# Optimization experiments

Hardware: AMD Instinct MI355X
Metric: run time of the kernel (lower is better)

## Reference

```python
import jax, jax.numpy as jnp
import numpy as np

TEMPERATURE = 0.1

def setup_inputs() -> dict:
    key = jax.random.key(0)
    k1, k2 = jax.random.split(key)
    z_i = jax.random.normal(k1, (4096, 128), dtype=jnp.float32)
    z_j = jax.random.normal(k2, (4096, 128), dtype=jnp.float32)
    return {"z_i": z_i, "z_j": z_j}

def reference(z_i, z_j):
    n = z_i.shape[0]
    reps = jnp.concatenate([z_i, z_j], axis=0)              # (2N, D)
    # cosine similarity via normalize + GEMM (same math as broadcasted CosineSimilarity,
    # torch eps=1e-8 on the norm)
    norms = jnp.maximum(jnp.linalg.norm(reps, axis=1, keepdims=True), 1e-8)
    rn = reps / norms
    sim = rn @ rn.T                                          # (2N, 2N)
    l_pos = jnp.diagonal(sim, offset=n)                      # (N,)
    r_pos = jnp.diagonal(sim, offset=-n)                     # (N,)
    positives = jnp.concatenate([l_pos, r_pos])[:, None]     # (2N, 1)
    # NOTE: original code's mask bug makes `negatives` the FULL sim matrix
    logits = jnp.concatenate([positives, sim], axis=1) / TEMPERATURE  # (2N, 2N+1)
    # cross-entropy with label 0, reduction='sum'
    log_probs = jax.nn.log_softmax(logits, axis=1)
    loss = -jnp.sum(log_probs[:, 0])
    return loss / (2 * n)
```

## Files before the change

### kernel.cpp

```cpp
#include <hip/hip_runtime.h>
#include <hip/hip_bf16.h>

typedef __bf16 bf16x8 __attribute__((ext_vector_type(8)));
typedef __bf16 bf16x2 __attribute__((ext_vector_type(2)));
typedef float f32x4 __attribute__((ext_vector_type(4)));

#define NROWS 8192
#define HALF_N 4096
#define DIM 128
#define ROW_BYTES 256
#define C1 14.42695040888963f
#define LN2 0.6931471805599453f

__global__ __launch_bounds__(256) void k_normalize(
    const float* __restrict__ zi, const float* __restrict__ zj,
    char* __restrict__ rn, char* __restrict__ rnA, float* __restrict__ rowsum)
{
    const int wave = threadIdx.x >> 6;
    const int lane = threadIdx.x & 63;
    #pragma unroll
    for (int i = 0; i < 4; ++i) {
        const int row = blockIdx.x * 16 + wave * 4 + i;
        const float* src = (row < HALF_N) ? (zi + (size_t)row * DIM)
                                          : (zj + (size_t)(row - HALF_N) * DIM);
        float2 v = *(const float2*)(src + lane * 2);
        float ss = v.x * v.x + v.y * v.y;
        #pragma unroll
        for (int m = 32; m >= 1; m >>= 1) ss += __shfl_xor(ss, m, 64);
        const float sc = 1.0f / fmaxf(sqrtf(ss), 1e-8f);
        bf16x2 a, b;
        a[0] = (__bf16)(v.x * sc);      a[1] = (__bf16)(v.y * sc);
        b[0] = (__bf16)(v.x * sc * C1); b[1] = (__bf16)(v.y * sc * C1);
        *(bf16x2*)(rn  + (size_t)row * ROW_BYTES + lane * 4) = a;
        *(bf16x2*)(rnA + (size_t)row * ROW_BYTES + lane * 4) = b;
    }
    if (threadIdx.x < 16) rowsum[blockIdx.x * 16 + threadIdx.x] = 0.0f;
}

__global__ __launch_bounds__(256) void k_gemm(
    const char* __restrict__ rn, const char* __restrict__ rnA,
    float* __restrict__ rowsum)
{
    const int wave = threadIdx.x >> 6;
    const int lane = threadIdx.x & 63;
    const int qrow = lane >> 4, lcol = lane & 15;
    const int cv = blockIdx.x & 15;
    const int rg = (blockIdx.x >> 4) * 4 + wave;

    const char* Ab = rnA + (size_t)(rg * 64) * ROW_BYTES;
    bf16x8 afrag[4][4];
    #pragma unroll
    for (int mi = 0; mi < 4; ++mi)
        #pragma unroll
        for (int ks = 0; ks < 4; ++ks)
            afrag[mi][ks] = *(const bf16x8*)(Ab + (mi * 16 + lcol) * ROW_BYTES
                                             + ks * 64 + qrow * 16);

    float rsum[4][4];
    #pragma unroll
    for (int mi = 0; mi < 4; ++mi)
        #pragma unroll
        for (int r = 0; r < 4; ++r) rsum[mi][r] = 0.0f;

    const char* Bb = rn + (size_t)(cv * 512) * ROW_BYTES + lcol * ROW_BYTES + qrow * 16;

    #pragma unroll 1
    for (int s = 0; s < 32; ++s) {
        const char* bp = Bb + s * 16 * ROW_BYTES;
        bf16x8 bfrag[4];
        #pragma unroll
        for (int ks = 0; ks < 4; ++ks)
            bfrag[ks] = *(const bf16x8*)(bp + ks * 64);

        f32x4 acc[4];
        const f32x4 zero = {0.0f, 0.0f, 0.0f, 0.0f};
        #pragma unroll
        for (int mi = 0; mi < 4; ++mi) acc[mi] = zero;
        #pragma unroll
        for (int ks = 0; ks < 4; ++ks)
            #pragma unroll
            for (int mi = 0; mi < 4; ++mi)
                acc[mi] = __builtin_amdgcn_mfma_f32_16x16x32_bf16(
                    afrag[mi][ks], bfrag[ks], acc[mi], 0, 0, 0);

        #pragma unroll
        for (int mi = 0; mi < 4; ++mi)
            #pragma unroll
            for (int r = 0; r < 4; ++r)
                rsum[mi][r] += __builtin_amdgcn_exp2f(acc[mi][r]);
    }

    #pragma unroll
    for (int mi = 0; mi < 4; ++mi)
        #pragma unroll
        for (int r = 0; r < 4; ++r) {
            float v = rsum[mi][r];
            v += __shfl_xor(v, 1, 64);
            v += __shfl_xor(v, 2, 64);
            v += __shfl_xor(v, 4, 64);
            v += __shfl_xor(v, 8, 64);
            if (lcol == 0)
                atomicAdd(&rowsum[rg * 64 + mi * 16 + qrow * 4 + r], v);
        }
}

__global__ __launch_bounds__(256) void k_rowloss(
    const char* __restrict__ rn, const float* __restrict__ rowsum,
    float* __restrict__ row_loss)
{
    const int row  = blockIdx.x * 4 + (threadIdx.x >> 6);
    const int lane = threadIdx.x & 63;
    const int partner = (row + HALF_N) & (NROWS - 1);
    const bf16x2 a = *(const bf16x2*)(rn + (size_t)row * ROW_BYTES + lane * 4);
    const bf16x2 b = *(const bf16x2*)(rn + (size_t)partner * ROW_BYTES + lane * 4);
    float p = (float)a[0] * (float)b[0] + (float)a[1] * (float)b[1];
    #pragma unroll
    for (int m = 32; m >= 1; m >>= 1) p += __shfl_xor(p, m, 64);
    if (lane == 0) {
        const float pc = p * C1;
        const float S  = rowsum[row] + __builtin_amdgcn_exp2f(pc);
        row_loss[row] = (__builtin_amdgcn_logf(S) - pc) * LN2;
    }
}

__global__ __launch_bounds__(256) void k_reduce(
    const float* __restrict__ row_loss, float* __restrict__ out)
{
    const f32x4* v4 = (const f32x4*)row_loss;
    float s = 0.0f;
    for (int i = threadIdx.x; i < NROWS / 4; i += 256) {
        f32x4 v = v4[i];
        s += (v[0] + v[1]) + (v[2] + v[3]);
    }
    #pragma unroll
    for (int m = 32; m >= 1; m >>= 1) s += __shfl_xor(s, m, 64);
    __shared__ float part[4];
    if ((threadIdx.x & 63) == 0) part[threadIdx.x >> 6] = s;
    __syncthreads();
    if (threadIdx.x == 0)
        out[0] = (part[0] + part[1] + part[2] + part[3]) * (1.0f / (float)NROWS);
}

extern "C" void kernel_launch(void* const* d_in, const int* in_sizes, int n_in,
                              void* d_out, int out_size, void* d_ws, size_t ws_size,
                              hipStream_t stream)
{
    const float* zi = (const float*)d_in[0];
    const float* zj = (const float*)d_in[1];
    float* out = (float*)d_out;

    char*  rn       = (char*)d_ws;
    char*  rnA      = rn + (size_t)NROWS * ROW_BYTES;
    float* rowsum   = (float*)(rnA + (size_t)NROWS * ROW_BYTES);
    float* row_loss = rowsum + NROWS;

    k_normalize<<<NROWS / 16, 256, 0, stream>>>(zi, zj, rn, rnA, rowsum);
    k_gemm<<<512, 256, 0, stream>>>(rn, rnA, rowsum);
    k_rowloss<<<NROWS / 4, 256, 0, stream>>>(rn, rowsum, row_loss);
    k_reduce<<<1, 256, 0, stream>>>(row_loss, out);
}
```

Baseline: 102.9 us.

## Fuse rowloss and reduce into GEMM via last-block pattern, halve GEMM tile

Normalization now processes z_i/z_j row pairs together and computes the positive-pair cosine directly into a buffer, removing the separate rowloss kernel. The GEMM grid doubles to 1024 blocks, each wave handling 32 rows instead of 64, and B fragments are double-buffered across iterations. A global atomic counter lets the last finishing block compute per-row losses and the final mean, eliminating two kernel launches. This trades launch overhead for an atomic fence and a serial tail in one block, and the positive logit now uses fp32 values instead of bf16.

```diff
diff --git a/kernel.cpp b/kernel.cpp
--- a/kernel.cpp
+++ b/kernel.cpp
@@ -11,35 +11,55 @@
 #define ROW_BYTES 256
 #define C1 14.42695040888963f
 #define LN2 0.6931471805599453f
+#define GBLK 1024
 
 __global__ __launch_bounds__(256) void k_normalize(
     const float* __restrict__ zi, const float* __restrict__ zj,
-    char* __restrict__ rn, char* __restrict__ rnA, float* __restrict__ rowsum)
+    char* __restrict__ rn, char* __restrict__ rnA,
+    float* __restrict__ rowsum, float* __restrict__ pbuf,
+    unsigned int* __restrict__ done)
 {
     const int wave = threadIdx.x >> 6;
     const int lane = threadIdx.x & 63;
     #pragma unroll
-    for (int i = 0; i < 4; ++i) {
-        const int row = blockIdx.x * 16 + wave * 4 + i;
-        const float* src = (row < HALF_N) ? (zi + (size_t)row * DIM)
-                                          : (zj + (size_t)(row - HALF_N) * DIM);
-        float2 v = *(const float2*)(src + lane * 2);
-        float ss = v.x * v.x + v.y * v.y;
+    for (int t = 0; t < 2; ++t) {
+        const int idx = blockIdx.x * 8 + wave * 2 + t;
+        float2 vi = *(const float2*)(zi + (size_t)idx * DIM + lane * 2);
+        float2 vj = *(const float2*)(zj + (size_t)idx * DIM + lane * 2);
+        float ssi = vi.x * vi.x + vi.y * vi.y;
+        float ssj = vj.x * vj.x + vj.y * vj.y;
+        float cr  = vi.x * vj.x + vi.y * vj.y;
         #pragma unroll
-        for (int m = 32; m >= 1; m >>= 1) ss += __shfl_xor(ss, m, 64);
-        const float sc = 1.0f / fmaxf(sqrtf(ss), 1e-8f);
+        for (int m = 32; m >= 1; m >>= 1) {
+            ssi += __shfl_xor(ssi, m, 64);
+            ssj += __shfl_xor(ssj, m, 64);
+            cr  += __shfl_xor(cr,  m, 64);
+        }
+        const float sci = 1.0f / fmaxf(sqrtf(ssi), 1e-8f);
+        const float scj = 1.0f / fmaxf(sqrtf(ssj), 1e-8f);
         bf16x2 a, b;
-        a[0] = (__bf16)(v.x * sc);      a[1] = (__bf16)(v.y * sc);
-        b[0] = (__bf16)(v.x * sc * C1); b[1] = (__bf16)(v.y * sc * C1);
-        *(bf16x2*)(rn  + (size_t)row * ROW_BYTES + lane * 4) = a;
-        *(bf16x2*)(rnA + (size_t)row * ROW_BYTES + lane * 4) = b;
+        a[0] = (__bf16)(vi.x * sci);      a[1] = (__bf16)(vi.y * sci);
+        b[0] = (__bf16)(vi.x * sci * C1); b[1] = (__bf16)(vi.y * sci * C1);
+        *(bf16x2*)(rn  + (size_t)idx * ROW_BYTES + lane * 4) = a;
+        *(bf16x2*)(rnA + (size_t)idx * ROW_BYTES + lane * 4) = b;
+        a[0] = (__bf16)(vj.x * scj);      a[1] = (__bf16)(vj.y * scj);
+        b[0] = (__bf16)(vj.x * scj * C1); b[1] = (__bf16)(vj.y * scj * C1);
+        *(bf16x2*)(rn  + (size_t)(idx + HALF_N) * ROW_BYTES + lane * 4) = a;
+        *(bf16x2*)(rnA + (size_t)(idx + HALF_N) * ROW_BYTES + lane * 4) = b;
+        if (lane == 0) {
+            const float p = cr * sci * scj;
+            pbuf[idx] = p;
+            pbuf[idx + HALF_N] = p;
+        }
     }
     if (threadIdx.x < 16) rowsum[blockIdx.x * 16 + threadIdx.x] = 0.0f;
+    if (blockIdx.x == 0 && threadIdx.x == 0) *done = 0u;
 }
 
 __global__ __launch_bounds__(256) void k_gemm(
     const char* __restrict__ rn, const char* __restrict__ rnA,
-    float* __restrict__ rowsum)
+    float* __restrict__ rowsum, const float* __restrict__ pbuf,
+    unsigned int* __restrict__ done, float* __restrict__ out)
 {
     const int wave = threadIdx.x >> 6;
     const int lane = threadIdx.x & 63;
@@ -47,51 +67,69 @@
     const int cv = blockIdx.x & 15;
     const int rg = (blockIdx.x >> 4) * 4 + wave;
 
-    const char* Ab = rnA + (size_t)(rg * 64) * ROW_BYTES;
-    bf16x8 afrag[4][4];
+    const char* Ab = rnA + (size_t)(rg * 32) * ROW_BYTES;
+    bf16x8 afrag[2][4];
     #pragma unroll
-    for (int mi = 0; mi < 4; ++mi)
+    for (int mi = 0; mi < 2; ++mi)
         #pragma unroll
         for (int ks = 0; ks < 4; ++ks)
             afrag[mi][ks] = *(const bf16x8*)(Ab + (mi * 16 + lcol) * ROW_BYTES
                                              + ks * 64 + qrow * 16);
 
-    float rsum[4][4];
+    float rsum[2][4];
     #pragma unroll
-    for (int mi = 0; mi < 4; ++mi)
+    for (int mi = 0; mi < 2; ++mi)
         #pragma unroll
         for (int r = 0; r < 4; ++r) rsum[mi][r] = 0.0f;
 
     const char* Bb = rn + (size_t)(cv * 512) * ROW_BYTES + lcol * ROW_BYTES + qrow * 16;
 
+    bf16x8 b0[4], b1[4];
+    #pragma unroll
+    for (int ks = 0; ks < 4; ++ks) b0[ks] = *(const bf16x8*)(Bb + ks * 64);
+
+    const f32x4 zero = {0.0f, 0.0f, 0.0f, 0.0f};
     #pragma unroll 1
-    for (int s = 0; s < 32; ++s) {
-        const char* bp = Bb + s * 16 * ROW_BYTES;
-        bf16x8 bfrag[4];
+    for (int s = 0; s < 32; s += 2) {
+        const char* bp1 = Bb + (size_t)(s + 1) * 16 * ROW_BYTES;
         #pragma unroll
-        for (int ks = 0; ks < 4; ++ks)
-            bfrag[ks] = *(const bf16x8*)(bp + ks * 64);
+        for (int ks = 0; ks < 4; ++ks) b1[ks] = *(const bf16x8*)(bp1 + ks * 64);
 
-        f32x4 acc[4];
-        const f32x4 zero = {0.0f, 0.0f, 0.0f, 0.0f};
-        #pragma unroll
-        for (int mi = 0; mi < 4; ++mi) acc[mi] = zero;
+        f32x4 acc[2]; acc[0] = zero; acc[1] = zero;
         #pragma unroll
         for (int ks = 0; ks < 4; ++ks)
             #pragma unroll
-            for (int mi = 0; mi < 4; ++mi)
+            for (int mi = 0; mi < 2; ++mi)
                 acc[mi] = __builtin_amdgcn_mfma_f32_16x16x32_bf16(
-                    afrag[mi][ks], bfrag[ks], acc[mi], 0, 0, 0);
+                    afrag[mi][ks], b0[ks], acc[mi], 0, 0, 0);
+        #pragma unroll
+        for (int mi = 0; mi < 2; ++mi)
+            #pragma unroll
+            for (int r = 0; r < 4; ++r)
+                rsum[mi][r] += __builtin_amdgcn_exp2f(acc[mi][r]);
 
+        if (s + 2 < 32) {
+            const char* bp2 = Bb + (size_t)(s + 2) * 16 * ROW_BYTES;
+            #pragma unroll
+            for (int ks = 0; ks < 4; ++ks) b0[ks] = *(const bf16x8*)(bp2 + ks * 64);
+        }
+
+        acc[0] = zero; acc[1] = zero;
         #pragma unroll
-        for (int mi = 0; mi < 4; ++mi)
+        for (int ks = 0; ks < 4; ++ks)
+            #pragma unroll
+            for (int mi = 0; mi < 2; ++mi)
+                acc[mi] = __builtin_amdgcn_mfma_f32_16x16x32_bf16(
+                    afrag[mi][ks], b1[ks], acc[mi], 0, 0, 0);
+        #pragma unroll
+        for (int mi = 0; mi < 2; ++mi)
             #pragma unroll
             for (int r = 0; r < 4; ++r)
                 rsum[mi][r] += __builtin_amdgcn_exp2f(acc[mi][r]);
     }
 
     #pragma unroll
-    for (int mi = 0; mi < 4; ++mi)
+    for (int mi = 0; mi < 2; ++mi)
         #pragma unroll
         for (int r = 0; r < 4; ++r) {
             float v = rsum[mi][r];
@@ -100,42 +138,32 @@
             v += __shfl_xor(v, 4, 64);
             v += __shfl_xor(v, 8, 64);
             if (lcol == 0)
-                atomicAdd(&rowsum[rg * 64 + mi * 16 + qrow * 4 + r], v);
+                atomicAdd(&rowsum[rg * 32 + mi * 16 + qrow * 4 + r], v);
         }
-}
 
-__global__ __launch_bounds__(256) void k_rowloss(
-    const char* __restrict__ rn, const float* __restrict__ rowsum,
-    float* __restrict__ row_loss)
-{
-    const int row  = blockIdx.x * 4 + (threadIdx.x >> 6);
-    const int lane = threadIdx.x & 63;
-    const int partner = (row + HALF_N) & (NROWS - 1);
-    const bf16x2 a = *(const bf16x2*)(rn + (size_t)row * ROW_BYTES + lane * 4);
-    const bf16x2 b = *(const bf16x2*)(rn + (size_t)partner * ROW_BYTES + lane * 4);
-    float p = (float)a[0] * (float)b[0] + (float)a[1] * (float)b[1];
-    #pragma unroll
-    for (int m = 32; m >= 1; m >>= 1) p += __shfl_xor(p, m, 64);
-    if (lane == 0) {
-        const float pc = p * C1;
-        const float S  = rowsum[row] + __builtin_amdgcn_exp2f(pc);
-        row_loss[row] = (__builtin_amdgcn_logf(S) - pc) * LN2;
+    __syncthreads();
+    __shared__ int is_last;
+    if (threadIdx.x == 0) {
+        __threadfence();
+        unsigned old = __hip_atomic_fetch_add(done, 1u, __ATOMIC_ACQ_REL,
+                                              __HIP_MEMORY_SCOPE_AGENT);
+        is_last = (old == GBLK - 1);
     }
-}
+    __syncthreads();
+    if (!is_last) return;
+    __threadfence();
 
-__global__ __launch_bounds__(256) void k_reduce(
-    const float* __restrict__ row_loss, float* __restrict__ out)
-{
-    const f32x4* v4 = (const f32x4*)row_loss;
-    float s = 0.0f;
-    for (int i = threadIdx.x; i < NROWS / 4; i += 256) {
-        f32x4 v = v4[i];
-        s += (v[0] + v[1]) + (v[2] + v[3]);
+    float lsum = 0.0f;
+    for (int r = threadIdx.x; r < NROWS; r += 256) {
+        float rs = __hip_atomic_load(&rowsum[r], __ATOMIC_RELAXED, __HIP_MEMORY_SCOPE_AGENT);
+        float pc = pbuf[r] * C1;
+        float S  = rs + __builtin_amdgcn_exp2f(pc);
+        lsum += (__builtin_amdgcn_logf(S) - pc) * LN2;
     }
     #pragma unroll
-    for (int m = 32; m >= 1; m >>= 1) s += __shfl_xor(s, m, 64);
+    for (int m = 32; m >= 1; m >>= 1) lsum += __shfl_xor(lsum, m, 64);
     __shared__ float part[4];
-    if ((threadIdx.x & 63) == 0) part[threadIdx.x >> 6] = s;
+    if (lane == 0) part[wave] = lsum;
     __syncthreads();
     if (threadIdx.x == 0)
         out[0] = (part[0] + part[1] + part[2] + part[3]) * (1.0f / (float)NROWS);
@@ -149,13 +177,12 @@
     const float* zj = (const float*)d_in[1];
     float* out = (float*)d_out;
 
-    char*  rn       = (char*)d_ws;
-    char*  rnA      = rn + (size_t)NROWS * ROW_BYTES;
-    float* rowsum   = (float*)(rnA + (size_t)NROWS * ROW_BYTES);
-    float* row_loss = rowsum + NROWS;
+    char*  rn     = (char*)d_ws;
+    char*  rnA    = rn + (size_t)NROWS * ROW_BYTES;
+    float* rowsum = (float*)(rnA + (size_t)NROWS * ROW_BYTES);
+    float* pbuf   = rowsum + NROWS;
+    unsigned int* done = (unsigned int*)(pbuf + NROWS);
 
-    k_normalize<<<NROWS / 16, 256, 0, stream>>>(zi, zj, rn, rnA, rowsum);
-    k_gemm<<<512, 256, 0, stream>>>(rn, rnA, rowsum);
-    k_rowloss<<<NROWS / 4, 256, 0, stream>>>(rn, rowsum, row_loss);
-    k_reduce<<<1, 256, 0, stream>>>(row_loss, out);
+    k_normalize<<<NROWS / 16, 256, 0, stream>>>(zi, zj, rn, rnA, rowsum, pbuf, done);
+    k_gemm<<<GBLK, 256, 0, stream>>>(rn, rnA, rowsum, pbuf, done, out);
 }
```

After: 151.2 us. +46.9%, slower.
